# Performance work log

Hardware: AMD Instinct MI355X
Metric: run time of the kernel (lower is better)

## Reference

```python
import jax, jax.numpy as jnp
import numpy as np

B, H, W, C = 8, 256, 256, 32
WIN = 8
HEADS = 2
DH = C // HEADS          # 16
HIDDEN = 128             # mlp_ratio * C
N = WIN * WIN            # 64 tokens per window


def _rel_index(win):
    # standard Swin relative position index, computed once (static int constant)
    coords = np.stack(np.meshgrid(np.arange(win), np.arange(win), indexing='ij'))  # [2,w,w]
    coords = coords.reshape(2, -1)                                                  # [2,N]
    rel = (coords[:, :, None] - coords[:, None, :]).transpose(1, 2, 0)              # [N,N,2]
    rel[:, :, 0] += win - 1
    rel[:, :, 1] += win - 1
    rel[:, :, 0] *= 2 * win - 1
    return jnp.asarray(rel.sum(-1))                                                 # [N,N]

REL_IDX = _rel_index(WIN)


def setup_inputs() -> dict:
    key = jax.random.key(0)
    ks = jax.random.split(key, 10)
    rn = lambda k, s: jax.random.normal(k, s, jnp.float32) * 0.02
    return {
        'x': jax.random.normal(ks[0], (B, H * W, C), jnp.float32),
        'norm1_g': jnp.ones((C,), jnp.float32), 'norm1_b': jnp.zeros((C,), jnp.float32),
        'wq': rn(ks[1], (C, C)), 'bq': jnp.zeros((C,), jnp.float32),
        'wkv': rn(ks[2], (C, 2 * C)), 'bkv': jnp.zeros((2 * C,), jnp.float32),
        'wo': rn(ks[3], (C, C)), 'bo': jnp.zeros((C,), jnp.float32),
        'rel_bias': rn(ks[4], ((2 * WIN - 1) ** 2, HEADS)),
        'norm2_g': jnp.ones((C,), jnp.float32), 'norm2_b': jnp.zeros((C,), jnp.float32),
        'w1': rn(ks[5], (C, HIDDEN)), 'b1': jnp.zeros((HIDDEN,), jnp.float32),
        'dw': rn(ks[6], (HIDDEN, 1, 3, 3)), 'dwb': jnp.zeros((HIDDEN,), jnp.float32),
        'w2': rn(ks[7], (HIDDEN, C)), 'b2': jnp.zeros((C,), jnp.float32),
    }


def _ln(x, g, b):
    mu = x.mean(-1, keepdims=True)
    var = x.var(-1, keepdims=True)
    return (x - mu) / jnp.sqrt(var + 1e-5) * g + b


def _gelu(x):
    return jax.nn.gelu(x, approximate=False)  # torch nn.GELU is exact erf


def reference(x, norm1_g, norm1_b, wq, bq, wkv, bkv, wo, bo, rel_bias,
              norm2_g, norm2_b, w1, b1, dw, dwb, w2, b2):
    shortcut = x                                              # [B, HW, C]
    xn = _ln(x, norm1_g, norm1_b).reshape(B, H, W, C)
    # window partition -> [B*nW, N, C]
    xw = (xn.reshape(B, H // WIN, WIN, W // WIN, WIN, C)
            .transpose(0, 1, 3, 2, 4, 5)
            .reshape(-1, N, C))
    # linear qkv projection
    q = (xw @ wq + bq).reshape(-1, N, HEADS, DH).transpose(0, 2, 1, 3)      # [B_,h,N,d]
    kv = (xw @ wkv + bkv).reshape(-1, N, 2, HEADS, DH).transpose(2, 0, 3, 1, 4)
    k, v = kv[0], kv[1]
    scale = DH ** -0.5
    attn = jnp.einsum('bhnd,bhmd->bhnm', q * scale, k)                      # [B_,h,N,N]
    bias = rel_bias[REL_IDX].transpose(2, 0, 1)                             # [h,N,N]
    attn = jax.nn.softmax(attn + bias[None], axis=-1)
    out = jnp.einsum('bhnm,bhmd->bhnd', attn, v).transpose(0, 2, 1, 3).reshape(-1, N, C)
    out = out @ wo + bo
    # window reverse -> [B, HW, C]
    out = (out.reshape(B, H // WIN, W // WIN, WIN, WIN, C)
              .transpose(0, 1, 3, 2, 4, 5)
              .reshape(B, H * W, C))
    x = shortcut + out
    # LeFF: linear -> dwconv3x3 over full HxW map -> linear
    y = _ln(x, norm2_g, norm2_b)
    y = _gelu(y @ w1 + b1)                                                  # [B,HW,HIDDEN]
    y = y.reshape(B, H, W, HIDDEN).transpose(0, 3, 1, 2)                    # NCHW
    y = jax.lax.conv_general_dilated(
        y, dw, window_strides=(1, 1), padding='SAME',
        dimension_numbers=('NCHW', 'OIHW', 'NCHW'), feature_group_count=HIDDEN)
    y = _gelu(y + dwb[None, :, None, None])
    y = y.transpose(0, 2, 3, 1).reshape(B, H * W, HIDDEN)
    y = y @ w2 + b2
    return x + y
```

## Files before the change

### kernel.cpp

```cpp
#include <hip/hip_runtime.h>
#include <hip/hip_bf16.h>
#include <math.h>

#define IMG   256
#define HWTOK 65536
#define CH    32

typedef __attribute__((ext_vector_type(8))) _Float16 half8v;
typedef __attribute__((ext_vector_type(2))) _Float16 half2v;
typedef __attribute__((ext_vector_type(4))) float floatx4;

__device__ __forceinline__ unsigned short f2h(float f) {
    _Float16 h = (_Float16)f;
    return __builtin_bit_cast(unsigned short, h);
}
__device__ __forceinline__ float h2f(unsigned short u) {
    return (float)__builtin_bit_cast(_Float16, u);
}
__device__ __forceinline__ unsigned packh2(float a, float b) {
    return (unsigned)f2h(a) | ((unsigned)f2h(b) << 16);
}

__device__ __forceinline__ half2v gelu2v(half2v v) {
    const half2v hi = (half2v)(_Float16)( 2.0f);
    const half2v lo = (half2v)(_Float16)(-2.0f);
    const half2v vc = __builtin_elementwise_min(__builtin_elementwise_max(v, lo), hi);
    const half2v s  = vc * vc;
    half2v p = s * (half2v)(_Float16)(-1.18726e-3f) + (half2v)(_Float16)(9.97356e-3f);
    p = s * p + (half2v)(_Float16)(-6.64904e-2f);
    p = s * p + (half2v)(_Float16)( 3.989423e-1f);
    return v * (vc * p + (half2v)(_Float16)(0.5f));
}

__global__ __launch_bounds__(128) void attn_kernel(
    const float* __restrict__ x,
    const float* __restrict__ n1g, const float* __restrict__ n1b,
    const float* __restrict__ wq,  const float* __restrict__ bq,
    const float* __restrict__ wkv, const float* __restrict__ bkv,
    const float* __restrict__ wo,  const float* __restrict__ bo,
    const float* __restrict__ relb,
    const float* __restrict__ w1,  const float* __restrict__ w2,
    unsigned short* __restrict__ w1p, unsigned short* __restrict__ w2p,
    float* __restrict__ x1)
{
    if (blockIdx.x >= 8192) {
        #pragma unroll
        for (int i = 0; i < 32; ++i) {
            const int t = threadIdx.x + i * 128;
            const int row = t >> 5, k = t & 31;
            const int bl = row >> 5, wi = row & 31;
            const int j = bl * 32 + ((wi & 15) << 1) + (wi >> 4);
            w1p[t] = f2h(w1[k * 128 + j]);
            const int n = t >> 7, kk = t & 127;
            w2p[t] = f2h(w2[kk * 32 + n]);
        }
        return;
    }

    struct Win {
        union {
            unsigned short xn[64][40];
            unsigned short P[2][64][72];
            unsigned short O[64][40];
        } u;
        unsigned short Q[64][40];
        unsigned short K[64][56];
        unsigned short VT[2][16][72];
    };
    __shared__ Win S;
    __shared__ unsigned short bias16[2][228];
    __shared__ float denom[2][64];

    const int tid = threadIdx.x;
    const int h   = tid >> 6;
    const int l   = tid & 63;
    const int lm  = l & 15, lq = l >> 4;

    const int win = blockIdx.x;
    const int b   = win >> 10;
    const int wh  = (win >> 5) & 31, ww = win & 31;
    const size_t wbase = ((size_t)b * HWTOK + (wh * 8) * IMG + ww * 8) * CH;

    const float LOG2E = 1.4426950408889634f;
    const float QSC   = 0.25f * LOG2E;

    half8v bwq, bwk, bwv, bwo0, bwo1;
    {
        const int lq8 = lq * 8;
        #pragma unroll
        for (int i = 0; i < 8; ++i) {
            bwq[i]  = (_Float16)(wq[(lq8 + i) * 32 + h * 16 + lm] * QSC);
            bwk[i]  = (_Float16)wkv[(lq8 + i) * 64 + h * 16 + lm];
            bwv[i]  = (_Float16)wkv[(lq8 + i) * 64 + 32 + h * 16 + lm];
            bwo0[i] = (_Float16)wo [(lq8 + i) * 32 + lm];
            bwo1[i] = (_Float16)wo [(lq8 + i) * 32 + 16 + lm];
        }
    }

    if (tid < 64) {
        const int st = tid;
        const size_t sbase = wbase + (size_t)((st >> 3) * IMG + (st & 7)) * CH;
        const float4* xp = (const float4*)(x + sbase);
        float xr[32];
        float mu = 0.f;
        #pragma unroll
        for (int i = 0; i < 8; ++i) {
            const float4 v = xp[i];
            xr[i*4+0]=v.x; xr[i*4+1]=v.y; xr[i*4+2]=v.z; xr[i*4+3]=v.w;
            mu += v.x + v.y + v.z + v.w;
        }
        mu *= (1.f / 32.f);
        float var = 0.f;
        #pragma unroll
        for (int c = 0; c < 32; ++c) { const float d = xr[c] - mu; var += d * d; }
        const float inv = rsqrtf(var * (1.f / 32.f) + 1e-5f);
        unsigned int pk[16];
        #pragma unroll
        for (int j = 0; j < 16; ++j)
            pk[j] = packh2((xr[2*j]   - mu) * inv * n1g[2*j]   + n1b[2*j],
                           (xr[2*j+1] - mu) * inv * n1g[2*j+1] + n1b[2*j+1]);
        uint4* dst = (uint4*)&S.u.xn[st][0];
        #pragma unroll
        for (int j = 0; j < 4; ++j) dst[j] = *(uint4*)&pk[j * 4];
        const uint4 z = {0u, 0u, 0u, 0u};
        *(uint4*)&S.K[st][16] = z;
        *(uint4*)&S.K[st][24] = z;
    } else {
        const int t2 = tid - 64;
        for (int i = t2; i < 450; i += 64) {
            const int hh = (i >= 225), r = i - hh * 225;
            bias16[hh][r] = f2h(relb[r * 2 + hh] * LOG2E);
        }
    }
    __syncthreads();

    const float bqv = bq[h*16 + lm] * QSC;
    const float bkv_ = bkv[h*16 + lm];
    const float bvv = bkv[32 + h*16 + lm];
    const floatx4 cq = {bqv, bqv, bqv, bqv};
    const floatx4 ck = {bkv_, bkv_, bkv_, bkv_};
    const floatx4 cv = {bvv, bvv, bvv, bvv};
    const floatx4 zero = {0.f, 0.f, 0.f, 0.f};

    #pragma unroll
    for (int mt = 0; mt < 4; ++mt) {
        const half8v a = *(const half8v*)&S.u.xn[mt*16 + lm][lq*8];
        const floatx4 dq = __builtin_amdgcn_mfma_f32_16x16x32_f16(a, bwq, cq, 0,0,0);
        const floatx4 dk = __builtin_amdgcn_mfma_f32_16x16x32_f16(a, bwk, ck, 0,0,0);
        const floatx4 dv = __builtin_amdgcn_mfma_f32_16x16x32_f16(a, bwv, cv, 0,0,0);
        const int r0 = mt*16 + lq*4;
        #pragma unroll
        for (int r = 0; r < 4; ++r) {
            S.Q[r0 + r][h*16 + lm] = f2h(dq[r]);
            S.K[r0 + r][h*32 + lm] = f2h(dk[r]);
        }
        uint2 vv;
        vv.x = packh2(dv[0], dv[1]);
        vv.y = packh2(dv[2], dv[3]);
        *(uint2*)&S.VT[h][lm][r0] = vv;
    }
    __syncthreads();

    half8v ak[4], bqf[4];
    #pragma unroll
    for (int mt = 0; mt < 4; ++mt)
        ak[mt] = *(const half8v*)&S.K[mt*16 + lm][h*16 + lq*8];
    #pragma unroll
    for (int nt = 0; nt < 4; ++nt)
        bqf[nt] = *(const half8v*)&S.Q[nt*16 + lm][lq*8];

    const int cc0 = (lm >> 3) * 15 + (lm & 7);
    const int cml = 15 * (lq >> 1) + 4 * (lq & 1);

    #pragma unroll
    for (int nt = 0; nt < 4; ++nt) {
        float sum = 0.f;
        const int base_nt = 30*nt + cc0 + 112 - cml;
        #pragma unroll
        for (int mt = 0; mt < 4; ++mt) {
            const floatx4 d = __builtin_amdgcn_mfma_f32_16x16x32_f16(ak[mt], bqf[nt], zero, 0,0,0);
            const int ib = base_nt - 30*mt;
            const float e0 = exp2f(d[0] + h2f(bias16[h][ib]));
            const float e1 = exp2f(d[1] + h2f(bias16[h][ib - 1]));
            const float e2 = exp2f(d[2] + h2f(bias16[h][ib - 2]));
            const float e3 = exp2f(d[3] + h2f(bias16[h][ib - 3]));
            sum += (e0 + e1) + (e2 + e3);
            uint2 pw;
            pw.x = packh2(e0, e1);
            pw.y = packh2(e2, e3);
            *(uint2*)&S.u.P[h][nt*16 + lm][mt*16 + lq*4] = pw;
        }
        sum += __shfl_xor(sum, 16);
        sum += __shfl_xor(sum, 32);
        if (l < 16) denom[h][nt*16 + l] = __frcp_rn(sum);
    }

    const half8v bva = *(const half8v*)&S.VT[h][lm][lq*8];
    const half8v bvb = *(const half8v*)&S.VT[h][lm][32 + lq*8];
    float oreg[16];
    #pragma unroll
    for (int mt = 0; mt < 4; ++mt) {
        const half8v ap0 = *(const half8v*)&S.u.P[h][mt*16 + lm][lq*8];
        const half8v ap1 = *(const half8v*)&S.u.P[h][mt*16 + lm][32 + lq*8];
        floatx4 ov = __builtin_amdgcn_mfma_f32_16x16x32_f16(ap0, bva, zero, 0,0,0);
        ov         = __builtin_amdgcn_mfma_f32_16x16x32_f16(ap1, bvb, ov,   0,0,0);
        const float4 dn = *(const float4*)&denom[h][mt*16 + lq*4];
        oreg[mt*4+0] = ov[0] * dn.x;
        oreg[mt*4+1] = ov[1] * dn.y;
        oreg[mt*4+2] = ov[2] * dn.z;
        oreg[mt*4+3] = ov[3] * dn.w;
    }
    __syncthreads();

    #pragma unroll
    for (int mt = 0; mt < 4; ++mt)
        #pragma unroll
        for (int r = 0; r < 4; ++r)
            S.u.O[mt*16 + lq*4 + r][h*16 + lm] = f2h(oreg[mt*4 + r]);
    __syncthreads();

    const float bo0 = bo[lm], bo1 = bo[16 + lm];
    const floatx4 co0 = {bo0, bo0, bo0, bo0};
    const floatx4 co1 = {bo1, bo1, bo1, bo1};
    #pragma unroll
    for (int mi = 0; mi < 2; ++mi) {
        const int mt = 2*h + mi;
        const half8v aO = *(const half8v*)&S.u.O[mt*16 + lm][lq*8];
        const floatx4 d0 = __builtin_amdgcn_mfma_f32_16x16x32_f16(aO, bwo0, co0, 0,0,0);
        const floatx4 d1 = __builtin_amdgcn_mfma_f32_16x16x32_f16(aO, bwo1, co1, 0,0,0);
        #pragma unroll
        for (int r = 0; r < 4; ++r) {
            const int t = mt*16 + lq*4 + r;
            const size_t g = wbase + (size_t)((t >> 3) * IMG + (t & 7)) * CH;
            x1[g + lm]      = x[g + lm]      + d0[r];
            x1[g + 16 + lm] = x[g + 16 + lm] + d1[r];
        }
    }
}

__global__ __launch_bounds__(256, 3) void leff_kernel_gw(
    const float* __restrict__ x1,
    const float* __restrict__ n2g, const float* __restrict__ n2b,
    const float* __restrict__ b1,
    const float* __restrict__ dw,  const float* __restrict__ dwb,
    const float* __restrict__ b2,
    const unsigned short* __restrict__ w1p,
    const unsigned short* __restrict__ w2p,
    float* __restrict__ out)
{
    __shared__ __align__(16) unsigned short xnA[112][40];
    union HG {
        unsigned short hid[100][128];
        unsigned short glA[64][132];
    };
    __shared__ __align__(16) HG hg;

    const int blk = blockIdx.x;
    const int b = blk >> 10, tyb = (blk >> 5) & 31, txb = blk & 31;
    const int y0 = tyb * 8, x0 = txb * 8;
    const int tid = threadIdx.x;
    const int wv = tid >> 6;
    const int l  = tid & 63;
    const int lm = l & 15;
    const int lq = l >> 4;
    const bool edge = (tyb == 0) | (tyb == 31) | (txb == 0) | (txb == 31);

    const half8v bf0 = *(const half8v*)&w1p[(wv * 32 + lm) * 32 + lq * 8];
    const half8v bf1 = *(const half8v*)&w1p[(wv * 32 + 16 + lm) * 32 + lq * 8];

    if (tid < 200) {
        const int px = tid >> 1, half = tid & 1;
        const int hy = px / 10, hx = px % 10;
        const int iy = y0 + hy - 1, ix = x0 + hx - 1;
        const bool inb = (iy >= 0 && iy < IMG && ix >= 0 && ix < IMG);
        unsigned int pk[8];
        if (inb) {
            const size_t base = ((size_t)b * HWTOK + iy * IMG + ix) * CH + half * 16;
            const float4* xp = (const float4*)(x1 + base);
            float v[16];
            float s = 0.f;
            #pragma unroll
            for (int i = 0; i < 4; ++i) {
                const float4 t = xp[i];
                v[i*4+0]=t.x; v[i*4+1]=t.y; v[i*4+2]=t.z; v[i*4+3]=t.w;
                s += t.x + t.y + t.z + t.w;
            }
            const float mu = (s + __shfl_xor(s, 1)) * (1.f / 32.f);
            float q = 0.f;
            #pragma unroll
            for (int c = 0; c < 16; ++c) { const float d = v[c]-mu; q += d*d; }
            const float var = q + __shfl_xor(q, 1);
            const float inv = rsqrtf(var * (1.f/32.f) + 1e-5f);
            #pragma unroll
            for (int j = 0; j < 8; ++j) {
                const int c = half*16 + 2*j;
                pk[j] = packh2((v[2*j]   - mu) * inv * n2g[c]   + n2b[c],
                               (v[2*j+1] - mu) * inv * n2g[c+1] + n2b[c+1]);
            }
        } else {
            #pragma unroll
            for (int j = 0; j < 8; ++j) pk[j] = 0u;
        }
        uint4* dst = (uint4*)&xnA[px][half * 16];
        dst[0] = *(uint4*)&pk[0];
        dst[1] = *(uint4*)&pk[4];
    } else if (tid < 248) {
        const int t2 = tid - 200;
        const uint4 z = {0u,0u,0u,0u};
        *(uint4*)&xnA[100 + (t2 >> 2)][(t2 & 3) * 8] = z;
    }
    __syncthreads();

    {
        const int c0 = wv * 32 + 2 * lm;
        const float bias0 = b1[c0], bias1 = b1[c0 + 1];
        const floatx4 cb0 = {bias0, bias0, bias0, bias0};
        const floatx4 cb1 = {bias1, bias1, bias1, bias1};
        for (int mt = 0; mt < 7; ++mt) {
            const half8v af = *(const half8v*)&xnA[mt * 16 + lm][lq * 8];
            floatx4 a0 = __builtin_amdgcn_mfma_f32_16x16x32_f16(af, bf0, cb0, 0, 0, 0);
            floatx4 a1 = __builtin_amdgcn_mfma_f32_16x16x32_f16(af, bf1, cb1, 0, 0, 0);
            #pragma unroll
            for (int r = 0; r < 4; ++r) {
                const int p = mt * 16 + lq * 4 + r;
                if (mt < 6 || p < 100) {
                    half2v hv;
                    hv.x = (_Float16)a0[r];
                    hv.y = (_Float16)a1[r];
                    half2v g = gelu2v(hv);
                    unsigned int bits = __builtin_bit_cast(unsigned int, g);
                    if (edge) {
                        const int hy = (p * 205) >> 11;
                        const int hx = p - hy * 10;
                        const int iy = y0 + hy - 1, ix = x0 + hx - 1;
                        const bool inb = (iy >= 0) & (iy < IMG) & (ix >= 0) & (ix < IMG);
                        if (!inb) bits = 0u;
                    }
                    *(unsigned int*)&hg.hid[p][c0] = bits;
                }
            }
        }
    }
    __syncthreads();

    {
        const int jq = tid & 31, pg = tid >> 5;
        const int j0 = 4 * jq;
        half2v dwa[9], dwc[9];
        #pragma unroll
        for (int t = 0; t < 9; ++t) {
            dwa[t].x = (_Float16)dw[(j0    ) * 9 + t];
            dwa[t].y = (_Float16)dw[(j0 + 1) * 9 + t];
            dwc[t].x = (_Float16)dw[(j0 + 2) * 9 + t];
            dwc[t].y = (_Float16)dw[(j0 + 3) * 9 + t];
        }
        half2v acca[8], accc[8];
        {
            half2v dba, dbc;
            dba.x = (_Float16)dwb[j0];     dba.y = (_Float16)dwb[j0 + 1];
            dbc.x = (_Float16)dwb[j0 + 2]; dbc.y = (_Float16)dwb[j0 + 3];
            #pragma unroll
            for (int i = 0; i < 8; ++i) { acca[i] = dba; accc[i] = dbc; }
        }
        #pragma unroll
        for (int ky = 0; ky < 3; ++ky) {
            uint2 rr[10];
            #pragma unroll
            for (int cx = 0; cx < 10; ++cx)
                rr[cx] = *(const uint2*)&hg.hid[(pg + ky) * 10 + cx][j0];
            #pragma unroll
            for (int i = 0; i < 8; ++i)
                #pragma unroll
                for (int kx = 0; kx < 3; ++kx) {
                    acca[i] = __builtin_bit_cast(half2v, rr[i + kx].x) * dwa[ky*3+kx] + acca[i];
                    accc[i] = __builtin_bit_cast(half2v, rr[i + kx].y) * dwc[ky*3+kx] + accc[i];
                }
        }
        __syncthreads();
        #pragma unroll
        for (int i = 0; i < 8; ++i) {
            const half2v ga = gelu2v(acca[i]);
            const half2v gc = gelu2v(accc[i]);
            uint2 ow;
            ow.x = __builtin_bit_cast(unsigned int, ga);
            ow.y = __builtin_bit_cast(unsigned int, gc);
            *(uint2*)&hg.glA[pg * 8 + i][j0] = ow;
        }
    }
    __syncthreads();

    {
        half8v w2f[2][4];
        #pragma unroll
        for (int nt = 0; nt < 2; ++nt)
            #pragma unroll
            for (int kc = 0; kc < 4; ++kc)
                w2f[nt][kc] = *(const half8v*)&w2p[(nt*16 + lm) * 128 + kc*32 + lq*8];
        #pragma unroll
        for (int nt = 0; nt < 2; ++nt) {
            const int mt = wv;
            const int c = nt * 16 + lm;
            const float bias = b2[c];
            floatx4 acc = {bias, bias, bias, bias};
            #pragma unroll
            for (int kc = 0; kc < 4; ++kc) {
                const half8v a = *(const half8v*)&hg.glA[mt * 16 + lm][kc * 32 + lq * 8];
                acc = __builtin_amdgcn_mfma_f32_16x16x32_f16(a, w2f[nt][kc], acc, 0, 0, 0);
            }
            #pragma unroll
            for (int r = 0; r < 4; ++r) {
                const int p = mt * 16 + lq * 4 + r;
                const int iy = y0 + (p >> 3), ix = x0 + (p & 7);
                const size_t g = ((size_t)b * HWTOK + iy * IMG + ix) * CH + c;
                out[g] = x1[g] + acc[r];
            }
        }
    }
}

extern "C" void kernel_launch(void* const* d_in, const int* in_sizes, int n_in,
                              void* d_out, int out_size, void* d_ws, size_t ws_size,
                              hipStream_t stream)
{
    const float* x    = (const float*)d_in[0];
    const float* n1g  = (const float*)d_in[1];
    const float* n1b  = (const float*)d_in[2];
    const float* wq   = (const float*)d_in[3];
    const float* bq   = (const float*)d_in[4];
    const float* wkv  = (const float*)d_in[5];
    const float* bkv  = (const float*)d_in[6];
    const float* wo   = (const float*)d_in[7];
    const float* bo   = (const float*)d_in[8];
    const float* relb = (const float*)d_in[9];
    const float* n2g  = (const float*)d_in[10];
    const float* n2b  = (const float*)d_in[11];
    const float* w1   = (const float*)d_in[12];
    const float* b1   = (const float*)d_in[13];
    const float* dw   = (const float*)d_in[14];
    const float* dwb  = (const float*)d_in[15];
    const float* w2   = (const float*)d_in[16];
    const float* b2   = (const float*)d_in[17];

    float* out = (float*)d_out;
    float* x1  = (float*)d_ws;
    const size_t X1_BYTES = (size_t)8 * HWTOK * CH * 4;
    unsigned short* w1p = (unsigned short*)((char*)d_ws + X1_BYTES);
    unsigned short* w2p = w1p + 4096;

    attn_kernel<<<8193, 128, 0, stream>>>(x, n1g, n1b, wq, bq, wkv, bkv,
                                          wo, bo, relb, w1, w2, w1p, w2p, x1);
    leff_kernel_gw<<<8192, 256, 0, stream>>>(x1, n2g, n2b, b1, dw, dwb,
                                             b2, w1p, w2p, out);
}
```

Measured before the change: 156.5 us.

## Move weight and bias preprocessing into a separate prep kernel with pre-packed layouts

Adds a small prep kernel that converts wq/wkv/wo, the depthwise weights and biases to fp16 in MFMA-friendly layouts, and expands the relative-position bias into per-lane float4 tiles. The attention kernel then loads weights as vector half8 loads and feeds the bias as the MFMA accumulator init, which removes the per-block strided scalar weight loads, the shared-memory bias table and the bias adds. LayerNorm is split across two threads per token, so all 128 threads work instead of 64. fp16 conversions now use the packed cvt_pkrtz instruction. The cost is one extra kernel launch and an extra global read of the expanded bias (about 32 KB) per block.

```diff
diff --git a/kernel.cpp b/kernel.cpp
--- a/kernel.cpp
+++ b/kernel.cpp
@@ -14,11 +14,11 @@
     _Float16 h = (_Float16)f;
     return __builtin_bit_cast(unsigned short, h);
 }
-__device__ __forceinline__ float h2f(unsigned short u) {
-    return (float)__builtin_bit_cast(_Float16, u);
+__device__ __forceinline__ half2v pkrtz(float a, float b) {
+    return __builtin_bit_cast(half2v, __builtin_amdgcn_cvt_pkrtz(a, b));
 }
 __device__ __forceinline__ unsigned packh2(float a, float b) {
-    return (unsigned)f2h(a) | ((unsigned)f2h(b) << 16);
+    return __builtin_bit_cast(unsigned, __builtin_amdgcn_cvt_pkrtz(a, b));
 }
 
 __device__ __forceinline__ half2v gelu2v(half2v v) {
@@ -32,31 +32,71 @@
     return v * (vc * p + (half2v)(_Float16)(0.5f));
 }
 
+__global__ __launch_bounds__(256) void prep_kernel(
+    const float* __restrict__ w1, const float* __restrict__ w2,
+    const float* __restrict__ wq, const float* __restrict__ wkv,
+    const float* __restrict__ wo, const float* __restrict__ dw,
+    const float* __restrict__ dwb, const float* __restrict__ relb,
+    unsigned short* __restrict__ w1p, unsigned short* __restrict__ w2p,
+    unsigned short* __restrict__ wqp, unsigned short* __restrict__ wkp,
+    unsigned short* __restrict__ wvp, unsigned short* __restrict__ wop,
+    unsigned short* __restrict__ dwp, unsigned short* __restrict__ dwbp,
+    float* __restrict__ biasf)
+{
+    const float LOG2E = 1.4426950408889634f;
+    const float QSC   = 0.25f * LOG2E;
+    const int bid = blockIdx.x, tid = threadIdx.x;
+
+    if (bid < 16) {
+        const int t = bid * 256 + tid;
+        const int row = t >> 5, k = t & 31;
+        const int bl = row >> 5, wi = row & 31;
+        const int j = bl * 32 + ((wi & 15) << 1) + (wi >> 4);
+        w1p[t] = f2h(w1[k * 128 + j]);
+        const int n = t >> 7, kk = t & 127;
+        w2p[t] = f2h(w2[kk * 32 + n]);
+    } else if (bid < 20) {
+        const int u = (bid - 16) * 256 + tid;
+        const int h = u >> 9, rem = u & 511;
+        const int col = rem >> 5, k = rem & 31;
+        wqp[u] = f2h(wq [k * 32 + h * 16 + col] * QSC);
+        wkp[u] = f2h(wkv[k * 64 + h * 16 + col]);
+        wvp[u] = f2h(wkv[k * 64 + 32 + h * 16 + col]);
+        const int n = u >> 5, kk2 = u & 31;
+        wop[u] = f2h(wo[kk2 * 32 + n]);
+    } else if (bid < 28) {
+        const int g = (bid - 20) * 256 + tid;
+        const int h = g >> 10, nt = (g >> 8) & 3, mt = (g >> 6) & 3, l = g & 63;
+        const int q = nt * 16 + (l & 15);
+        const int mb = mt * 16 + (l >> 4) * 4;
+        const int qy = q >> 3, qx = q & 7;
+        #pragma unroll
+        for (int r = 0; r < 4; ++r) {
+            const int m = mb + r;
+            const int my = m >> 3, mx = m & 7;
+            const int idx = (qy - my + 7) * 15 + (qx - mx + 7);
+            biasf[g * 4 + r] = relb[idx * 2 + h] * LOG2E;
+        }
+    } else {
+        for (int e = tid; e < 1280; e += 256) {
+            if (e < 1152) dwp[e] = f2h(dw[(e & 127) * 9 + (e >> 7)]);
+            else          dwbp[e - 1152] = f2h(dwb[e - 1152]);
+        }
+    }
+}
+
 __global__ __launch_bounds__(128) void attn_kernel(
     const float* __restrict__ x,
     const float* __restrict__ n1g, const float* __restrict__ n1b,
-    const float* __restrict__ wq,  const float* __restrict__ bq,
-    const float* __restrict__ wkv, const float* __restrict__ bkv,
-    const float* __restrict__ wo,  const float* __restrict__ bo,
-    const float* __restrict__ relb,
-    const float* __restrict__ w1,  const float* __restrict__ w2,
-    unsigned short* __restrict__ w1p, unsigned short* __restrict__ w2p,
+    const float* __restrict__ bq,  const float* __restrict__ bkv,
+    const float* __restrict__ bo,
+    const unsigned short* __restrict__ wqp,
+    const unsigned short* __restrict__ wkp,
+    const unsigned short* __restrict__ wvp,
+    const unsigned short* __restrict__ wop,
+    const float4* __restrict__ biasf4,
     float* __restrict__ x1)
 {
-    if (blockIdx.x >= 8192) {
-        #pragma unroll
-        for (int i = 0; i < 32; ++i) {
-            const int t = threadIdx.x + i * 128;
-            const int row = t >> 5, k = t & 31;
-            const int bl = row >> 5, wi = row & 31;
-            const int j = bl * 32 + ((wi & 15) << 1) + (wi >> 4);
-            w1p[t] = f2h(w1[k * 128 + j]);
-            const int n = t >> 7, kk = t & 127;
-            w2p[t] = f2h(w2[kk * 32 + n]);
-        }
-        return;
-    }
-
     struct Win {
         union {
             unsigned short xn[64][40];
@@ -64,11 +104,10 @@
             unsigned short O[64][40];
         } u;
         unsigned short Q[64][40];
-        unsigned short K[64][56];
+        unsigned short K[64][48];
         unsigned short VT[2][16][72];
     };
     __shared__ Win S;
-    __shared__ unsigned short bias16[2][228];
     __shared__ float denom[2][64];
 
     const int tid = threadIdx.x;
@@ -84,53 +123,43 @@
     const float LOG2E = 1.4426950408889634f;
     const float QSC   = 0.25f * LOG2E;
 
-    half8v bwq, bwk, bwv, bwo0, bwo1;
+    const half8v bwq  = *(const half8v*)&wqp[h * 512 + lm * 32 + lq * 8];
+    const half8v bwk  = *(const half8v*)&wkp[h * 512 + lm * 32 + lq * 8];
+    const half8v bwv  = *(const half8v*)&wvp[h * 512 + lm * 32 + lq * 8];
+    const half8v bwo0 = *(const half8v*)&wop[lm * 32 + lq * 8];
+    const half8v bwo1 = *(const half8v*)&wop[(16 + lm) * 32 + lq * 8];
+
     {
-        const int lq8 = lq * 8;
-        #pragma unroll
-        for (int i = 0; i < 8; ++i) {
-            bwq[i]  = (_Float16)(wq[(lq8 + i) * 32 + h * 16 + lm] * QSC);
-            bwk[i]  = (_Float16)wkv[(lq8 + i) * 64 + h * 16 + lm];
-            bwv[i]  = (_Float16)wkv[(lq8 + i) * 64 + 32 + h * 16 + lm];
-            bwo0[i] = (_Float16)wo [(lq8 + i) * 32 + lm];
-            bwo1[i] = (_Float16)wo [(lq8 + i) * 32 + 16 + lm];
-        }
-    }
-
-    if (tid < 64) {
-        const int st = tid;
-        const size_t sbase = wbase + (size_t)((st >> 3) * IMG + (st & 7)) * CH;
+        const int tok = tid >> 1, half = tid & 1;
+        const size_t sbase = wbase
+            + (size_t)((tok >> 3) * IMG + (tok & 7)) * CH + half * 16;
         const float4* xp = (const float4*)(x + sbase);
-        float xr[32];
-        float mu = 0.f;
-        #pragma unroll
-        for (int i = 0; i < 8; ++i) {
-            const float4 v = xp[i];
-            xr[i*4+0]=v.x; xr[i*4+1]=v.y; xr[i*4+2]=v.z; xr[i*4+3]=v.w;
-            mu += v.x + v.y + v.z + v.w;
-        }
-        mu *= (1.f / 32.f);
-        float var = 0.f;
-        #pragma unroll
-        for (int c = 0; c < 32; ++c) { const float d = xr[c] - mu; var += d * d; }
+        float v[16];
+        float s = 0.f;
+        #pragma unroll
+        for (int i = 0; i < 4; ++i) {
+            const float4 t = xp[i];
+            v[i*4+0]=t.x; v[i*4+1]=t.y; v[i*4+2]=t.z; v[i*4+3]=t.w;
+            s += t.x + t.y + t.z + t.w;
+        }
+        const float mu = (s + __shfl_xor(s, 1)) * (1.f / 32.f);
+        float qq = 0.f;
+        #pragma unroll
+        for (int c = 0; c < 16; ++c) { const float d = v[c] - mu; qq += d * d; }
+        const float var = qq + __shfl_xor(qq, 1);
         const float inv = rsqrtf(var * (1.f / 32.f) + 1e-5f);
-        unsigned int pk[16];
-        #pragma unroll
-        for (int j = 0; j < 16; ++j)
-            pk[j] = packh2((xr[2*j]   - mu) * inv * n1g[2*j]   + n1b[2*j],
-                           (xr[2*j+1] - mu) * inv * n1g[2*j+1] + n1b[2*j+1]);
-        uint4* dst = (uint4*)&S.u.xn[st][0];
-        #pragma unroll
-        for (int j = 0; j < 4; ++j) dst[j] = *(uint4*)&pk[j * 4];
+        unsigned pk[8];
+        #pragma unroll
+        for (int j = 0; j < 8; ++j) {
+            const int c = half * 16 + 2 * j;
+            pk[j] = packh2((v[2*j]   - mu) * inv * n1g[c]   + n1b[c],
+                           (v[2*j+1] - mu) * inv * n1g[c+1] + n1b[c+1]);
+        }
+        uint4* dst = (uint4*)&S.u.xn[tok][half * 16];
+        dst[0] = *(uint4*)&pk[0];
+        dst[1] = *(uint4*)&pk[4];
         const uint4 z = {0u, 0u, 0u, 0u};
-        *(uint4*)&S.K[st][16] = z;
-        *(uint4*)&S.K[st][24] = z;
-    } else {
-        const int t2 = tid - 64;
-        for (int i = t2; i < 450; i += 64) {
-            const int hh = (i >= 225), r = i - hh * 225;
-            bias16[hh][r] = f2h(relb[r * 2 + hh] * LOG2E);
-        }
+        *(uint4*)&S.K[tok][16 + half * 8] = z;
     }
     __syncthreads();
 
@@ -169,21 +198,18 @@
     for (int nt = 0; nt < 4; ++nt)
         bqf[nt] = *(const half8v*)&S.Q[nt*16 + lm][lq*8];
 
-    const int cc0 = (lm >> 3) * 15 + (lm & 7);
-    const int cml = 15 * (lq >> 1) + 4 * (lq & 1);
-
     #pragma unroll
     for (int nt = 0; nt < 4; ++nt) {
         float sum = 0.f;
-        const int base_nt = 30*nt + cc0 + 112 - cml;
         #pragma unroll
         for (int mt = 0; mt < 4; ++mt) {
-            const floatx4 d = __builtin_amdgcn_mfma_f32_16x16x32_f16(ak[mt], bqf[nt], zero, 0,0,0);
-            const int ib = base_nt - 30*mt;
-            const float e0 = exp2f(d[0] + h2f(bias16[h][ib]));
-            const float e1 = exp2f(d[1] + h2f(bias16[h][ib - 1]));
-            const float e2 = exp2f(d[2] + h2f(bias16[h][ib - 2]));
-            const float e3 = exp2f(d[3] + h2f(bias16[h][ib - 3]));
+            const float4 cb = biasf4[(h*16 + nt*4 + mt) * 64 + l];
+            const floatx4 C = {cb.x, cb.y, cb.z, cb.w};
+            const floatx4 d = __builtin_amdgcn_mfma_f32_16x16x32_f16(ak[mt], bqf[nt], C, 0,0,0);
+            const float e0 = exp2f(d[0]);
+            const float e1 = exp2f(d[1]);
+            const float e2 = exp2f(d[2]);
+            const float e3 = exp2f(d[3]);
             sum += (e0 + e1) + (e2 + e3);
             uint2 pw;
             pw.x = packh2(e0, e1);
@@ -241,11 +267,11 @@
 __global__ __launch_bounds__(256, 3) void leff_kernel_gw(
     const float* __restrict__ x1,
     const float* __restrict__ n2g, const float* __restrict__ n2b,
-    const float* __restrict__ b1,
-    const float* __restrict__ dw,  const float* __restrict__ dwb,
-    const float* __restrict__ b2,
+    const float* __restrict__ b1,  const float* __restrict__ b2,
     const unsigned short* __restrict__ w1p,
     const unsigned short* __restrict__ w2p,
+    const unsigned short* __restrict__ dwp,
+    const unsigned short* __restrict__ dwbp,
     float* __restrict__ out)
 {
     __shared__ __align__(16) unsigned short xnA[112][40];
@@ -324,10 +350,7 @@
             for (int r = 0; r < 4; ++r) {
                 const int p = mt * 16 + lq * 4 + r;
                 if (mt < 6 || p < 100) {
-                    half2v hv;
-                    hv.x = (_Float16)a0[r];
-                    hv.y = (_Float16)a1[r];
-                    half2v g = gelu2v(hv);
+                    half2v g = gelu2v(pkrtz(a0[r], a1[r]));
                     unsigned int bits = __builtin_bit_cast(unsigned int, g);
                     if (edge) {
                         const int hy = (p * 205) >> 11;
@@ -349,16 +372,15 @@
         half2v dwa[9], dwc[9];
         #pragma unroll
         for (int t = 0; t < 9; ++t) {
-            dwa[t].x = (_Float16)dw[(j0    ) * 9 + t];
-            dwa[t].y = (_Float16)dw[(j0 + 1) * 9 + t];
-            dwc[t].x = (_Float16)dw[(j0 + 2) * 9 + t];
-            dwc[t].y = (_Float16)dw[(j0 + 3) * 9 + t];
+            const uint2 wp = *(const uint2*)&dwp[t * 128 + j0];
+            dwa[t] = __builtin_bit_cast(half2v, wp.x);
+            dwc[t] = __builtin_bit_cast(half2v, wp.y);
         }
         half2v acca[8], accc[8];
         {
-            half2v dba, dbc;
-            dba.x = (_Float16)dwb[j0];     dba.y = (_Float16)dwb[j0 + 1];
-            dbc.x = (_Float16)dwb[j0 + 2]; dbc.y = (_Float16)dwb[j0 + 3];
+            const uint2 bp = *(const uint2*)&dwbp[j0];
+            const half2v dba = __builtin_bit_cast(half2v, bp.x);
+            const half2v dbc = __builtin_bit_cast(half2v, bp.y);
             #pragma unroll
             for (int i = 0; i < 8; ++i) { acca[i] = dba; accc[i] = dbc; }
         }
@@ -443,12 +465,23 @@
 
     float* out = (float*)d_out;
     float* x1  = (float*)d_ws;
-    const size_t X1_BYTES = (size_t)8 * HWTOK * CH * 4;
-    unsigned short* w1p = (unsigned short*)((char*)d_ws + X1_BYTES);
-    unsigned short* w2p = w1p + 4096;
-
-    attn_kernel<<<8193, 128, 0, stream>>>(x, n1g, n1b, wq, bq, wkv, bkv,
-                                          wo, bo, relb, w1, w2, w1p, w2p, x1);
-    leff_kernel_gw<<<8192, 256, 0, stream>>>(x1, n2g, n2b, b1, dw, dwb,
-                                             b2, w1p, w2p, out);
-}
+    char* base = (char*)d_ws + (size_t)8 * HWTOK * CH * 4;
+    unsigned short* w1p  = (unsigned short*)(base);
+    unsigned short* w2p  = (unsigned short*)(base + 8192);
+    unsigned short* wqp  = (unsigned short*)(base + 16384);
+    unsigned short* wkp  = (unsigned short*)(base + 18432);
+    unsigned short* wvp  = (unsigned short*)(base + 20480);
+    unsigned short* wop  = (unsigned short*)(base + 22528);
+    unsigned short* dwp  = (unsigned short*)(base + 24576);
+    unsigned short* dwbp = (unsigned short*)(base + 26880);
+    float*          bias = (float*)(base + 28672);
+
+    prep_kernel<<<29, 256, 0, stream>>>(w1, w2, wq, wkv, wo, dw, dwb, relb,
+                                        w1p, w2p, wqp, wkp, wvp, wop,
+                                        dwp, dwbp, bias);
+    attn_kernel<<<8192, 128, 0, stream>>>(x, n1g, n1b, bq, bkv, bo,
+                                          wqp, wkp, wvp, wop,
+                                          (const float4*)bias, x1);
+    leff_kernel_gw<<<8192, 256, 0, stream>>>(x1, n2g, n2b, b1, b2,
+                                             w1p, w2p, dwp, dwbp, out);
+}
```

Measured after the change: 140.3 us. -10.3%, faster.
